# Performance work log

Hardware: AMD Instinct MI355X
Metric: run time of the kernel (lower is better)

The kernel has to match this reference:

```python
import jax, jax.numpy as jnp
import numpy as np
import math

B, S, D_IN, D_ATTN, D_HID = 4, 2048, 1024, 1024, 1024

def gelu_erf(x):
    return 0.5 * x * (1.0 + jax.lax.erf(x / math.sqrt(2.0)))

def setup_inputs() -> dict:
    key = jax.random.key(0)
    k = jax.random.split(key, 8)
    inputs = jax.random.normal(k[0], (B, S, D_IN), dtype=jnp.float32)
    attn_mask = jax.random.randint(k[1], (B, S, S), 0, 2, dtype=jnp.int32)
    sq = 1.0 / math.sqrt(D_IN)
    Wq = jax.random.normal(k[2], (D_IN, D_ATTN), dtype=jnp.float32) * sq
    bq = jnp.zeros((D_ATTN,), dtype=jnp.float32)
    Wk = jax.random.normal(k[3], (D_IN, D_ATTN), dtype=jnp.float32) * sq
    bk = jnp.zeros((D_ATTN,), dtype=jnp.float32)
    Wv = jax.random.normal(k[4], (D_IN, D_HID), dtype=jnp.float32) * sq
    bv = jnp.zeros((D_HID,), dtype=jnp.float32)
    return {"inputs": inputs, "attn_mask": attn_mask,
            "Wq": Wq, "bq": bq, "Wk": Wk, "bk": bk, "Wv": Wv, "bv": bv}

def reference(inputs, attn_mask, Wq, bq, Wk, bk, Wv, bv):
    # Q, K: [B, S, d_k]
    Q = inputs @ Wq + bq
    K = inputs @ Wk + bk
    scores = jnp.einsum('bqd,bkd->bqk', Q, K) / math.sqrt(D_ATTN)
    scores = scores + attn_mask.astype(scores.dtype) * (-1e9)
    attn = jax.nn.softmax(scores, axis=-1)
    WV = gelu_erf(inputs @ Wv + bv)           # [B, S, hidden]
    context = jnp.einsum('bqk,bkh->bqh', attn, WV)
    return (context, attn)
```

## Files before the change

### kernel.cpp

```cpp
#include <hip/hip_runtime.h>
#include <hip/hip_bf16.h>
#include <math.h>

#define B_   4
#define S_   2048
#define DIN  1024
#define DATT 1024
#define DHID 1024

typedef short bf16x8 __attribute__((ext_vector_type(8)));
typedef float f32x4  __attribute__((ext_vector_type(4)));

__device__ inline unsigned short f2bf(float f) {
    unsigned u = __float_as_uint(f);
    u += 0x7fffu + ((u >> 16) & 1u);
    return (unsigned short)(u >> 16);
}
__device__ inline float bf2f(unsigned u16) {
    return __uint_as_float(u16 << 16);
}
__device__ inline void gld16(const void* g, void* l) {
    __builtin_amdgcn_global_load_lds(
        (const __attribute__((address_space(1))) unsigned int*)g,
        (__attribute__((address_space(3))) unsigned int*)l, 16, 0, 0);
}

__global__ __launch_bounds__(256)
void xcvt_k(const float* __restrict__ x, unsigned short* __restrict__ xb)
{
    int i = blockIdx.x * 256 + threadIdx.x;
    const float4* p = (const float4*)x + (size_t)i * 2;
    float4 v0 = p[0], v1 = p[1];
    uint4 o;
    o.x = (unsigned)f2bf(v0.x) | ((unsigned)f2bf(v0.y) << 16);
    o.y = (unsigned)f2bf(v0.z) | ((unsigned)f2bf(v0.w) << 16);
    o.z = (unsigned)f2bf(v1.x) | ((unsigned)f2bf(v1.y) << 16);
    o.w = (unsigned)f2bf(v1.z) | ((unsigned)f2bf(v1.w) << 16);
    ((uint4*)xb)[i] = o;
}

__global__ __launch_bounds__(256)
void wcvt_k(const float* __restrict__ Wq, const float* __restrict__ Wk,
            const float* __restrict__ Wv, unsigned short* __restrict__ Wt)
{
    int w = blockIdx.y;
    const float* W = (w == 0) ? Wq : ((w == 1) ? Wk : Wv);
    unsigned short* D = Wt + (size_t)w * DIN * DATT;
    int t = blockIdx.x * 256 + threadIdx.x;
    int n  = t >> 6;
    int kc = (t & 63) * 16;
    unsigned short r[16];
#pragma unroll
    for (int i = 0; i < 16; ++i) r[i] = f2bf(W[(size_t)(kc + i) * DATT + n]);
    uint4 o0, o1;
    o0.x = (unsigned)r[0] | ((unsigned)r[1] << 16);  o0.y = (unsigned)r[2] | ((unsigned)r[3] << 16);
    o0.z = (unsigned)r[4] | ((unsigned)r[5] << 16);  o0.w = (unsigned)r[6] | ((unsigned)r[7] << 16);
    o1.x = (unsigned)r[8] | ((unsigned)r[9] << 16);  o1.y = (unsigned)r[10] | ((unsigned)r[11] << 16);
    o1.z = (unsigned)r[12] | ((unsigned)r[13] << 16); o1.w = (unsigned)r[14] | ((unsigned)r[15] << 16);
    *(uint4*)(D + (size_t)n * DIN + kc)     = o0;
    *(uint4*)(D + (size_t)n * DIN + kc + 8) = o1;
}

template<int AMODE, int EPI>
__global__ __launch_bounds__(256)
void gemm_k(const void* __restrict__ Ap, const unsigned short* __restrict__ Bp,
            const float* __restrict__ b0, const float* __restrict__ b1,
            const float* __restrict__ b2, const int* __restrict__ maskp,
            void* __restrict__ Cp, void* __restrict__ Cp2,
            int K, int lda, int ldb, int ldc,
            long aStride, long bStride, long cStride, long mStride, float scale)
{
    __shared__ __align__(16) unsigned short sh[2][2][128][64];

    const int tid  = threadIdx.x;
    const int z    = blockIdx.z;
    const int row0 = blockIdx.y * 128;
    const int col0 = blockIdx.x * 128;
    const int wave = tid >> 6, lane = tid & 63;
    const int lr = lane & 15, lg = lane >> 4;
    const int wm = (wave >> 1) * 64, wn = (wave & 1) * 64;

    const unsigned short* Bb = Bp + (size_t)bStride * z;

    f32x4 acc[4][4] = {};
    const int nt = K >> 6;

    auto stage = [&](int b, int k0) {
        if (AMODE == 0) {
            const unsigned short* A = (const unsigned short*)Ap + (size_t)aStride * z;
#pragma unroll
            for (int q = 0; q < 4; ++q) {
                int c = q * 256 + tid;
                int row = c >> 3, j = c & 7;
                gld16((const char*)(A + (size_t)(row0 + row) * lda + k0) + ((j ^ (row & 7)) << 4),
                      (char*)&sh[b][0][0][0] + ((q * 256 + (tid & 192)) << 4));
            }
        } else {
            const float* A = (const float*)Ap + (size_t)aStride * z;
#pragma unroll
            for (int q = 0; q < 4; ++q) {
                int c = q * 256 + tid;
                int row = c >> 3, j = c & 7;
                const float* src = A + (size_t)(row0 + row) * lda + k0 + ((j ^ (row & 7)) << 3);
                float4 v0 = *(const float4*)src;
                float4 v1 = *(const float4*)(src + 4);
                uint4 p;
                p.x = (unsigned)f2bf(v0.x) | ((unsigned)f2bf(v0.y) << 16);
                p.y = (unsigned)f2bf(v0.z) | ((unsigned)f2bf(v0.w) << 16);
                p.z = (unsigned)f2bf(v1.x) | ((unsigned)f2bf(v1.y) << 16);
                p.w = (unsigned)f2bf(v1.z) | ((unsigned)f2bf(v1.w) << 16);
                *(uint4*)((char*)&sh[b][0][0][0] + ((size_t)c << 4)) = p;
            }
        }
#pragma unroll
        for (int q = 0; q < 4; ++q) {
            int c = q * 256 + tid;
            int row = c >> 3, j = c & 7;
            gld16((const char*)(Bb + (size_t)(col0 + row) * ldb + k0) + ((j ^ (row & 7)) << 4),
                  (char*)&sh[b][1][0][0] + ((q * 256 + (tid & 192)) << 4));
        }
    };

    stage(0, 0);
    __syncthreads();
    int cur = 0;
    for (int t = 0; t < nt; ++t) {
        if (t + 1 < nt) stage(cur ^ 1, (t + 1) << 6);
        const char* baseA = (const char*)&sh[cur][0][0][0];
        const char* baseB = (const char*)&sh[cur][1][0][0];
        bf16x8 af[2][4], bfv[2][4];
#pragma unroll
        for (int s = 0; s < 2; ++s)
#pragma unroll
            for (int i = 0; i < 4; ++i) {
                int ra = wm + i * 16 + lr;
                af[s][i]  = *(const bf16x8*)(baseA + ra * 128 + ((((s << 2) | lg) ^ (ra & 7)) << 4));
                int rb = wn + i * 16 + lr;
                bfv[s][i] = *(const bf16x8*)(baseB + rb * 128 + ((((s << 2) | lg) ^ (rb & 7)) << 4));
            }
#pragma unroll
        for (int s = 0; s < 2; ++s)
#pragma unroll
            for (int mi = 0; mi < 4; ++mi)
#pragma unroll
                for (int ni = 0; ni < 4; ++ni)
                    acc[mi][ni] = __builtin_amdgcn_mfma_f32_16x16x32_bf16(af[s][mi], bfv[s][ni], acc[mi][ni], 0, 0, 0);
        if (t + 1 < nt) __syncthreads();
        cur ^= 1;
    }

    if (EPI == 6) {
        int w = col0 >> 10;
        int cb = (col0 & 1023) + wn;
        if (w < 2) {
            unsigned short* C = (unsigned short*)Cp + (size_t)w * ((size_t)B_ * S_ * DATT);
            const float* bias = w ? b1 : b0;
#pragma unroll
            for (int mi = 0; mi < 4; ++mi)
#pragma unroll
                for (int ni = 0; ni < 4; ++ni) {
                    int col = cb + ni * 16 + lr;
                    float bb = bias[col];
                    int rowb = row0 + wm + mi * 16 + lg * 4;
#pragma unroll
                    for (int v = 0; v < 4; ++v)
                        C[(size_t)(rowb + v) * DATT + col] = f2bf(acc[mi][ni][v] + bb);
                }
        } else {
            unsigned short* C = (unsigned short*)Cp2;
            int zz = row0 >> 11;
            int sb = (row0 & 2047) + wm;
#pragma unroll
            for (int mi = 0; mi < 4; ++mi)
#pragma unroll
                for (int ni = 0; ni < 4; ++ni) {
                    int col = cb + ni * 16 + lr;
                    float bb = b2[col];
                    unsigned short r[4];
#pragma unroll
                    for (int v = 0; v < 4; ++v) {
                        float xv = acc[mi][ni][v] + bb;
                        xv = 0.5f * xv * (1.0f + erff(xv * 0.70710678118654752f));
                        r[v] = f2bf(xv);
                    }
                    uint2 o;
                    o.x = (unsigned)r[0] | ((unsigned)r[1] << 16);
                    o.y = (unsigned)r[2] | ((unsigned)r[3] << 16);
                    *(uint2*)(C + ((size_t)zz * DHID + col) * S_ + sb + mi * 16 + lg * 4) = o;
                }
        }
    } else if (EPI == 4) {
        unsigned short* C = (unsigned short*)Cp + (size_t)cStride * z;
        const int* mp = maskp + (size_t)mStride * z;
#pragma unroll
        for (int mi = 0; mi < 4; ++mi)
#pragma unroll
            for (int ni = 0; ni < 4; ++ni) {
                int col = col0 + wn + ni * 16 + lr;
                int rowb = row0 + wm + mi * 16 + lg * 4;
#pragma unroll
                for (int v = 0; v < 4; ++v) {
                    float sv = acc[mi][ni][v] * scale;
                    int mk = mp[(size_t)(rowb + v) * ldc + col];
                    float ev = mk ? 0.0f : __expf(sv);
                    C[(size_t)(rowb + v) * ldc + col] = f2bf(ev);
                }
            }
    } else if (EPI == 5) {
        float* C = (float*)Cp + (size_t)cStride * z;
        const float* invs = b0 + (size_t)z * S_;
#pragma unroll
        for (int mi = 0; mi < 4; ++mi)
#pragma unroll
            for (int ni = 0; ni < 4; ++ni) {
                int col = col0 + wn + ni * 16 + lr;
                int rowb = row0 + wm + mi * 16 + lg * 4;
#pragma unroll
                for (int v = 0; v < 4; ++v)
                    C[(size_t)(rowb + v) * ldc + col] = acc[mi][ni][v] * invs[rowb + v];
            }
    } else {
        float* C = (float*)Cp + (size_t)cStride * z;
        const int* mp = (EPI == 2) ? (maskp + (size_t)mStride * z) : nullptr;
#pragma unroll
        for (int mi = 0; mi < 4; ++mi)
#pragma unroll
            for (int ni = 0; ni < 4; ++ni) {
                int col = col0 + wn + ni * 16 + lr;
                int rowb = row0 + wm + mi * 16 + lg * 4;
#pragma unroll
                for (int v = 0; v < 4; ++v) {
                    float val = acc[mi][ni][v];
                    if (EPI == 2) val = val * scale + (float)mp[(size_t)(rowb + v) * ldc + col] * (-1e9f);
                    C[(size_t)(rowb + v) * ldc + col] = val;
                }
            }
    }
}

template<bool WRITEATTN>
__global__ __launch_bounds__(256)
void rownorm_k(const unsigned short* __restrict__ e, float* __restrict__ attn,
               float* __restrict__ invs)
{
    const int row = blockIdx.x;
    const int tid = threadIdx.x;
    uint4 u = ((const uint4*)(e + (size_t)row * S_))[tid];
    float f[8];
    f[0] = bf2f(u.x & 0xffffu); f[1] = bf2f(u.x >> 16);
    f[2] = bf2f(u.y & 0xffffu); f[3] = bf2f(u.y >> 16);
    f[4] = bf2f(u.z & 0xffffu); f[5] = bf2f(u.z >> 16);
    f[6] = bf2f(u.w & 0xffffu); f[7] = bf2f(u.w >> 16);
    float s = ((f[0] + f[1]) + (f[2] + f[3])) + ((f[4] + f[5]) + (f[6] + f[7]));
#pragma unroll
    for (int o = 32; o; o >>= 1) s += __shfl_xor(s, o);
    __shared__ float red[4];
    if ((tid & 63) == 0) red[tid >> 6] = s;
    __syncthreads();
    s = (red[0] + red[1]) + (red[2] + red[3]);
    float inv = 1.0f / s;
    if (WRITEATTN) {
        float* p = attn + (size_t)row * S_;
        ((float4*)p)[tid * 2]     = make_float4(f[0] * inv, f[1] * inv, f[2] * inv, f[3] * inv);
        ((float4*)p)[tid * 2 + 1] = make_float4(f[4] * inv, f[5] * inv, f[6] * inv, f[7] * inv);
    } else {
        if (tid == 0) invs[row] = inv;
    }
}

__global__ __launch_bounds__(256)
void softmax_k(float* __restrict__ attn)
{
    const int row = blockIdx.x;
    float* p = attn + (size_t)row * S_;
    const int tid = threadIdx.x;
    float4 a = ((const float4*)p)[tid * 2];
    float4 b = ((const float4*)p)[tid * 2 + 1];
    float m = fmaxf(fmaxf(fmaxf(a.x, a.y), fmaxf(a.z, a.w)),
                    fmaxf(fmaxf(b.x, b.y), fmaxf(b.z, b.w)));
#pragma unroll
    for (int o = 32; o; o >>= 1) m = fmaxf(m, __shfl_xor(m, o));
    __shared__ float redm[4];
    __shared__ float reds[4];
    if ((tid & 63) == 0) redm[tid >> 6] = m;
    __syncthreads();
    m = fmaxf(fmaxf(redm[0], redm[1]), fmaxf(redm[2], redm[3]));
    float e[8];
    e[0] = expf(a.x - m); e[1] = expf(a.y - m); e[2] = expf(a.z - m); e[3] = expf(a.w - m);
    e[4] = expf(b.x - m); e[5] = expf(b.y - m); e[6] = expf(b.z - m); e[7] = expf(b.w - m);
    float s = e[0] + e[1] + e[2] + e[3] + e[4] + e[5] + e[6] + e[7];
#pragma unroll
    for (int o = 32; o; o >>= 1) s += __shfl_xor(s, o);
    if ((tid & 63) == 0) reds[tid >> 6] = s;
    __syncthreads();
    s = reds[0] + reds[1] + reds[2] + reds[3];
    float inv = 1.0f / s;
    ((float4*)p)[tid * 2]     = make_float4(e[0] * inv, e[1] * inv, e[2] * inv, e[3] * inv);
    ((float4*)p)[tid * 2 + 1] = make_float4(e[4] * inv, e[5] * inv, e[6] * inv, e[7] * inv);
}

extern "C" void kernel_launch(void* const* d_in, const int* in_sizes, int n_in,
                              void* d_out, int out_size, void* d_ws, size_t ws_size,
                              hipStream_t stream)
{
    const float* x    = (const float*)d_in[0];
    const int*   mask = (const int*)d_in[1];
    const float* Wq   = (const float*)d_in[2];
    const float* bq   = (const float*)d_in[3];
    const float* Wk   = (const float*)d_in[4];
    const float* bk   = (const float*)d_in[5];
    const float* Wv   = (const float*)d_in[6];
    const float* bv   = (const float*)d_in[7];

    float* ctx  = (float*)d_out;
    float* attn = ctx + (size_t)B_ * S_ * DHID;

    unsigned short* Qb = (unsigned short*)ctx;
    unsigned short* Kb = Qb + (size_t)B_ * S_ * DATT;
    unsigned short* Xb   = (unsigned short*)attn;
    unsigned short* Wb   = Xb + (size_t)B_ * S_ * DIN;
    unsigned short* WVbT = Wb + (size_t)3 * DIN * DATT;

    const size_t eElems = (size_t)B_ * S_ * S_;
    bool fast = ws_size >= eElems * 2 + (size_t)B_ * S_ * 4 + 256;

    dim3 blk(256);

    xcvt_k<<<dim3(4096), blk, 0, stream>>>(x, Xb);
    wcvt_k<<<dim3(256, 3), blk, 0, stream>>>(Wq, Wk, Wv, Wb);

    if (fast) {
        unsigned short* e    = (unsigned short*)d_ws;
        float*          invs = (float*)(e + eElems);

        gemm_k<0, 6><<<dim3(24, 64, 1), blk, 0, stream>>>(
            Xb, Wb, bq, bk, bv, nullptr, Qb, WVbT,
            DIN, DIN, DIN, 0, 0, 0, 0, 0, 1.0f);
        gemm_k<0, 4><<<dim3(16, 16, 4), blk, 0, stream>>>(
            Qb, Kb, nullptr, nullptr, nullptr, mask, e, nullptr,
            DATT, DATT, DATT, S_,
            (long)S_ * DATT, (long)S_ * DATT, (long)S_ * S_, (long)S_ * S_, 0.03125f);
        rownorm_k<false><<<dim3(B_ * S_), blk, 0, stream>>>(e, nullptr, invs);
        gemm_k<0, 5><<<dim3(8, 16, 4), blk, 0, stream>>>(
            e, WVbT, invs, nullptr, nullptr, nullptr, ctx, nullptr,
            S_, S_, S_, DHID,
            (long)S_ * S_, (long)DHID * S_, (long)S_ * DHID, 0, 1.0f);
        rownorm_k<true><<<dim3(B_ * S_), blk, 0, stream>>>(e, attn, nullptr);
    } else {
        unsigned short* WVw = (unsigned short*)d_ws;
        gemm_k<0, 6><<<dim3(24, 64, 1), blk, 0, stream>>>(
            Xb, Wb, bq, bk, bv, nullptr, Qb, WVw,
            DIN, DIN, DIN, 0, 0, 0, 0, 0, 1.0f);
        gemm_k<0, 2><<<dim3(16, 16, 4), blk, 0, stream>>>(
            Qb, Kb, nullptr, nullptr, nullptr, mask, attn, nullptr,
            DATT, DATT, DATT, S_,
            (long)S_ * DATT, (long)S_ * DATT, (long)S_ * S_, (long)S_ * S_, 0.03125f);
        softmax_k<<<dim3(B_ * S_), blk, 0, stream>>>(attn);
        gemm_k<1, 3><<<dim3(8, 16, 4), blk, 0, stream>>>(
            attn, WVw, nullptr, nullptr, nullptr, nullptr, ctx, nullptr,
            S_, S_, S_, DHID,
            (long)S_ * S_, (long)DHID * S_, (long)S_ * DHID, 0, 1.0f);
    }
}
```

Measured before the change: 228.5 us.

## Add 256x256-tile, 8-wave GEMM kernel with phased LDS pipelining for fast path

Introduces a new GEMM kernel with 256x256 output tiles, 512 threads and 128KB of LDS double buffering. The main loop is split into four phases that interleave global-to-LDS prefetch with MFMA work, using explicit vmcnt waits, barriers and setprio. All three GEMMs on the fast path (QKV projection, masked exp scores, context) now use it, raising data reuse per loaded tile and reducing global traffic. The trade-off is fewer blocks (e.g. 256 for the score GEMM) and heavy register and LDS use, which can cut occupancy and leave CUs underused at wave tails.

```diff
diff --git a/kernel.cpp b/kernel.cpp
--- a/kernel.cpp
+++ b/kernel.cpp
@@ -61,6 +61,205 @@
     *(uint4*)(D + (size_t)n * DIN + kc + 8) = o1;
 }
 
+template<int EPI>
+__global__ __launch_bounds__(512, 2)
+void gemm256_k(const unsigned short* __restrict__ Ap, const unsigned short* __restrict__ Bp,
+               const float* __restrict__ b0, const float* __restrict__ b1,
+               const float* __restrict__ b2, const int* __restrict__ maskp,
+               void* __restrict__ Cp, void* __restrict__ Cp2,
+               int K, int lda, int ldb, int ldc,
+               long aStride, long bStride, long cStride, long mStride, float scale)
+{
+    __shared__ __align__(16) char ldsb[131072];
+
+    const int tid  = threadIdx.x;
+    const int z    = blockIdx.z;
+    const int row0 = blockIdx.y * 256;
+    const int col0 = blockIdx.x * 256;
+    const int wid  = tid >> 6, lane = tid & 63;
+    const int lr = lane & 15, lg = lane >> 4;
+    const int wm = wid >> 2, wn = wid & 3;
+    const int tw = (tid & 448) * 16;
+
+    const unsigned short* Ab = Ap + (size_t)aStride * z;
+    const unsigned short* Bb = Bp + (size_t)bStride * z;
+
+    const int swzA = lr & 7;
+    const int swzB = lg ^ ((lr >> 1) & 3);
+
+    f32x4 acc[8][4] = {};
+    const int nt = K >> 6;
+
+#define STAGE_A(buf, k0n, r) {                                                  \
+    int gr = (((r) & 1) << 7) + (((r) >> 1) << 6) + (tid >> 3);                 \
+    int jj = (tid & 7) ^ (gr & 7);                                              \
+    gld16(Ab + (size_t)(row0 + gr) * lda + (k0n) + jj * 8,                      \
+          ldsb + (size_t)(buf) * 65536 + (r) * 8192 + tw); }
+
+#define STAGE_B(buf, k0n, r) {                                                  \
+    int rw = (((r) & 1) << 7) + (tid >> 2);                                     \
+    int jj = (tid & 3) ^ ((rw >> 1) & 3);                                       \
+    gld16(Bb + (size_t)(col0 + rw) * ldb + (k0n) + ((r) >> 1) * 32 + jj * 8,    \
+          ldsb + (size_t)(buf) * 65536 + 32768 + ((r) >> 1) * 16384             \
+               + (((r) & 1) << 13) + tw); }
+
+#define PHASE(mh, kk, DOSTAGE) {                                                \
+    const char* lb = ldsb + (size_t)cb * 65536;                                 \
+    bf16x8 av[4], bv[4];                                                        \
+    _Pragma("unroll")                                                           \
+    for (int m = 0; m < 4; ++m) {                                               \
+        int Rl = (mh) * 128 + wm * 64 + m * 16 + lr;                            \
+        av[m] = *(const bf16x8*)(lb + Rl * 128 + ((((kk) * 4 + lg) ^ swzA) * 16)); \
+    }                                                                           \
+    _Pragma("unroll")                                                           \
+    for (int n = 0; n < 4; ++n) {                                               \
+        int Rb = wn * 64 + n * 16 + lr;                                         \
+        bv[n] = *(const bf16x8*)(lb + 32768 + (kk) * 16384 + Rb * 64 + swzB * 16); \
+    }                                                                           \
+    DOSTAGE;                                                                    \
+    asm volatile("s_waitcnt lgkmcnt(0)" ::: "memory");                          \
+    __builtin_amdgcn_sched_barrier(0);                                          \
+    __builtin_amdgcn_s_setprio(1);                                              \
+    _Pragma("unroll")                                                           \
+    for (int m = 0; m < 4; ++m)                                                 \
+        _Pragma("unroll")                                                       \
+        for (int n = 0; n < 4; ++n)                                             \
+            acc[(mh) * 4 + m][n] = __builtin_amdgcn_mfma_f32_16x16x32_bf16(     \
+                av[m], bv[n], acc[(mh) * 4 + m][n], 0, 0, 0);                   \
+    __builtin_amdgcn_s_setprio(0); }
+
+    STAGE_A(0, 0, 0); STAGE_B(0, 0, 0);
+    STAGE_A(0, 0, 1); STAGE_B(0, 0, 1);
+    STAGE_A(0, 0, 2); STAGE_A(0, 0, 3);
+    STAGE_B(0, 0, 2); STAGE_B(0, 0, 3);
+
+    int cb = 0;
+    for (int t = 0; t < nt; ++t) {
+        const bool pf = (t + 1) < nt;
+        const int k0n = (t + 1) << 6;
+        const int nb = cb ^ 1;
+        asm volatile("s_waitcnt vmcnt(4)\ns_barrier" ::: "memory");
+        PHASE(0, 0, if (pf) { STAGE_A(nb, k0n, 0); STAGE_B(nb, k0n, 0); })
+        if (pf) asm volatile("s_waitcnt vmcnt(4)\ns_barrier" ::: "memory");
+        else    asm volatile("s_waitcnt vmcnt(2)\ns_barrier" ::: "memory");
+        PHASE(1, 0, if (pf) { STAGE_A(nb, k0n, 1); STAGE_B(nb, k0n, 1); })
+        if (pf) asm volatile("s_waitcnt vmcnt(4)\ns_barrier" ::: "memory");
+        else    asm volatile("s_waitcnt vmcnt(0)\ns_barrier" ::: "memory");
+        PHASE(0, 1, if (pf) { STAGE_A(nb, k0n, 2); STAGE_A(nb, k0n, 3); })
+        PHASE(1, 1, if (pf) { STAGE_B(nb, k0n, 2); STAGE_B(nb, k0n, 3); })
+        cb = nb;
+    }
+#undef PHASE
+#undef STAGE_A
+#undef STAGE_B
+
+    if (EPI == 6) {
+        int w = col0 >> 10;
+        int cb0 = (col0 & 1023) + wn * 64;
+        if (w < 2) {
+            unsigned short* C = (unsigned short*)Cp + (size_t)w * ((size_t)B_ * S_ * DATT);
+            const float* bias = w ? b1 : b0;
+#pragma unroll
+            for (int ni = 0; ni < 4; ++ni) {
+                int col = cb0 + ni * 16 + lr;
+                float bb = bias[col];
+#pragma unroll
+                for (int mi = 0; mi < 8; ++mi) {
+                    int rowb = row0 + wm * 128 + mi * 16 + lg * 4;
+#pragma unroll
+                    for (int v = 0; v < 4; ++v)
+                        C[(size_t)(rowb + v) * DATT + col] = f2bf(acc[mi][ni][v] + bb);
+                }
+            }
+        } else {
+            unsigned short* C = (unsigned short*)Cp2;
+            int zz = row0 >> 11;
+            int sb = (row0 & 2047) + wm * 128;
+#pragma unroll
+            for (int ni = 0; ni < 4; ++ni) {
+                int col = cb0 + ni * 16 + lr;
+                float bb = b2[col];
+#pragma unroll
+                for (int mi = 0; mi < 8; ++mi) {
+                    unsigned short r[4];
+#pragma unroll
+                    for (int v = 0; v < 4; ++v) {
+                        float xv = acc[mi][ni][v] + bb;
+                        xv = 0.5f * xv * (1.0f + erff(xv * 0.70710678118654752f));
+                        r[v] = f2bf(xv);
+                    }
+                    uint2 o;
+                    o.x = (unsigned)r[0] | ((unsigned)r[1] << 16);
+                    o.y = (unsigned)r[2] | ((unsigned)r[3] << 16);
+                    *(uint2*)(C + ((size_t)zz * DHID + col) * S_ + sb + mi * 16 + lg * 4) = o;
+                }
+            }
+        }
+    } else if (EPI == 4) {
+        unsigned short* C = (unsigned short*)Cp + (size_t)cStride * z;
+        const int* mp = maskp + (size_t)mStride * z;
+#pragma unroll
+        for (int mi = 0; mi < 8; ++mi) {
+            int rowb = row0 + wm * 128 + mi * 16 + lg * 4;
+#pragma unroll
+            for (int ni = 0; ni < 4; ++ni) {
+                int col = col0 + wn * 64 + ni * 16 + lr;
+#pragma unroll
+                for (int v = 0; v < 4; ++v) {
+                    float sv = acc[mi][ni][v] * scale;
+                    int mk = mp[(size_t)(rowb + v) * ldc + col];
+                    float ev = mk ? 0.0f : __expf(sv);
+                    C[(size_t)(rowb + v) * ldc + col] = f2bf(ev);
+                }
+            }
+        }
+    } else {
+        float* C = (float*)Cp + (size_t)cStride * z;
+        const float* invs = b0 + (size_t)z * S_;
+#pragma unroll
+        for (int mi = 0; mi < 8; ++mi) {
+            int rowb = row0 + wm * 128 + mi * 16 + lg * 4;
+#pragma unroll
+            for (int ni = 0; ni < 4; ++ni) {
+                int col = col0 + wn * 64 + ni * 16 + lr;
+#pragma unroll
+                for (int v = 0; v < 4; ++v)
+                    C[(size_t)(rowb + v) * ldc + col] = acc[mi][ni][v] * invs[rowb + v];
+            }
+        }
+    }
+}
+
+template<bool WRITEATTN>
+__global__ __launch_bounds__(256)
+void rownorm_k(const unsigned short* __restrict__ e, float* __restrict__ attn,
+               float* __restrict__ invs)
+{
+    const int row = blockIdx.x;
+    const int tid = threadIdx.x;
+    uint4 u = ((const uint4*)(e + (size_t)row * S_))[tid];
+    float f[8];
+    f[0] = bf2f(u.x & 0xffffu); f[1] = bf2f(u.x >> 16);
+    f[2] = bf2f(u.y & 0xffffu); f[3] = bf2f(u.y >> 16);
+    f[4] = bf2f(u.z & 0xffffu); f[5] = bf2f(u.z >> 16);
+    f[6] = bf2f(u.w & 0xffffu); f[7] = bf2f(u.w >> 16);
+    float s = ((f[0] + f[1]) + (f[2] + f[3])) + ((f[4] + f[5]) + (f[6] + f[7]));
+#pragma unroll
+    for (int o = 32; o; o >>= 1) s += __shfl_xor(s, o);
+    __shared__ float red[4];
+    if ((tid & 63) == 0) red[tid >> 6] = s;
+    __syncthreads();
+    s = (red[0] + red[1]) + (red[2] + red[3]);
+    float inv = 1.0f / s;
+    if (WRITEATTN) {
+        float* p = attn + (size_t)row * S_;
+        ((float4*)p)[tid * 2]     = make_float4(f[0] * inv, f[1] * inv, f[2] * inv, f[3] * inv);
+        ((float4*)p)[tid * 2 + 1] = make_float4(f[4] * inv, f[5] * inv, f[6] * inv, f[7] * inv);
+    } else {
+        if (tid == 0) invs[row] = inv;
+    }
+}
+
 template<int AMODE, int EPI>
 __global__ __launch_bounds__(256)
 void gemm_k(const void* __restrict__ Ap, const unsigned short* __restrict__ Bp,
@@ -71,7 +270,6 @@
             long aStride, long bStride, long cStride, long mStride, float scale)
 {
     __shared__ __align__(16) unsigned short sh[2][2][128][64];
-
     const int tid  = threadIdx.x;
     const int z    = blockIdx.z;
     const int row0 = blockIdx.y * 128;
@@ -79,12 +277,9 @@
     const int wave = tid >> 6, lane = tid & 63;
     const int lr = lane & 15, lg = lane >> 4;
     const int wm = (wave >> 1) * 64, wn = (wave & 1) * 64;
-
     const unsigned short* Bb = Bp + (size_t)bStride * z;
-
     f32x4 acc[4][4] = {};
     const int nt = K >> 6;
-
     auto stage = [&](int b, int k0) {
         if (AMODE == 0) {
             const unsigned short* A = (const unsigned short*)Ap + (size_t)aStride * z;
@@ -120,7 +315,6 @@
                   (char*)&sh[b][1][0][0] + ((q * 256 + (tid & 192)) << 4));
         }
     };
-
     stage(0, 0);
     __syncthreads();
     int cur = 0;
@@ -148,7 +342,6 @@
         if (t + 1 < nt) __syncthreads();
         cur ^= 1;
     }
-
     if (EPI == 6) {
         int w = col0 >> 10;
         int cb = (col0 & 1023) + wn;
@@ -189,36 +382,6 @@
                     *(uint2*)(C + ((size_t)zz * DHID + col) * S_ + sb + mi * 16 + lg * 4) = o;
                 }
         }
-    } else if (EPI == 4) {
-        unsigned short* C = (unsigned short*)Cp + (size_t)cStride * z;
-        const int* mp = maskp + (size_t)mStride * z;
-#pragma unroll
-        for (int mi = 0; mi < 4; ++mi)
-#pragma unroll
-            for (int ni = 0; ni < 4; ++ni) {
-                int col = col0 + wn + ni * 16 + lr;
-                int rowb = row0 + wm + mi * 16 + lg * 4;
-#pragma unroll
-                for (int v = 0; v < 4; ++v) {
-                    float sv = acc[mi][ni][v] * scale;
-                    int mk = mp[(size_t)(rowb + v) * ldc + col];
-                    float ev = mk ? 0.0f : __expf(sv);
-                    C[(size_t)(rowb + v) * ldc + col] = f2bf(ev);
-                }
-            }
-    } else if (EPI == 5) {
-        float* C = (float*)Cp + (size_t)cStride * z;
-        const float* invs = b0 + (size_t)z * S_;
-#pragma unroll
-        for (int mi = 0; mi < 4; ++mi)
-#pragma unroll
-            for (int ni = 0; ni < 4; ++ni) {
-                int col = col0 + wn + ni * 16 + lr;
-                int rowb = row0 + wm + mi * 16 + lg * 4;
-#pragma unroll
-                for (int v = 0; v < 4; ++v)
-                    C[(size_t)(rowb + v) * ldc + col] = acc[mi][ni][v] * invs[rowb + v];
-            }
     } else {
         float* C = (float*)Cp + (size_t)cStride * z;
         const int* mp = (EPI == 2) ? (maskp + (size_t)mStride * z) : nullptr;
@@ -235,36 +398,6 @@
                     C[(size_t)(rowb + v) * ldc + col] = val;
                 }
             }
-    }
-}
-
-template<bool WRITEATTN>
-__global__ __launch_bounds__(256)
-void rownorm_k(const unsigned short* __restrict__ e, float* __restrict__ attn,
-               float* __restrict__ invs)
-{
-    const int row = blockIdx.x;
-    const int tid = threadIdx.x;
-    uint4 u = ((const uint4*)(e + (size_t)row * S_))[tid];
-    float f[8];
-    f[0] = bf2f(u.x & 0xffffu); f[1] = bf2f(u.x >> 16);
-    f[2] = bf2f(u.y & 0xffffu); f[3] = bf2f(u.y >> 16);
-    f[4] = bf2f(u.z & 0xffffu); f[5] = bf2f(u.z >> 16);
-    f[6] = bf2f(u.w & 0xffffu); f[7] = bf2f(u.w >> 16);
-    float s = ((f[0] + f[1]) + (f[2] + f[3])) + ((f[4] + f[5]) + (f[6] + f[7]));
-#pragma unroll
-    for (int o = 32; o; o >>= 1) s += __shfl_xor(s, o);
-    __shared__ float red[4];
-    if ((tid & 63) == 0) red[tid >> 6] = s;
-    __syncthreads();
-    s = (red[0] + red[1]) + (red[2] + red[3]);
-    float inv = 1.0f / s;
-    if (WRITEATTN) {
-        float* p = attn + (size_t)row * S_;
-        ((float4*)p)[tid * 2]     = make_float4(f[0] * inv, f[1] * inv, f[2] * inv, f[3] * inv);
-        ((float4*)p)[tid * 2 + 1] = make_float4(f[4] * inv, f[5] * inv, f[6] * inv, f[7] * inv);
-    } else {
-        if (tid == 0) invs[row] = inv;
     }
 }
 
@@ -324,7 +457,7 @@
     const size_t eElems = (size_t)B_ * S_ * S_;
     bool fast = ws_size >= eElems * 2 + (size_t)B_ * S_ * 4 + 256;
 
-    dim3 blk(256);
+    dim3 blk(256), blk5(512);
 
     xcvt_k<<<dim3(4096), blk, 0, stream>>>(x, Xb);
     wcvt_k<<<dim3(256, 3), blk, 0, stream>>>(Wq, Wk, Wv, Wb);
@@ -333,15 +466,15 @@
         unsigned short* e    = (unsigned short*)d_ws;
         float*          invs = (float*)(e + eElems);
 
-        gemm_k<0, 6><<<dim3(24, 64, 1), blk, 0, stream>>>(
+        gemm256_k<6><<<dim3(12, 32, 1), blk5, 0, stream>>>(
             Xb, Wb, bq, bk, bv, nullptr, Qb, WVbT,
             DIN, DIN, DIN, 0, 0, 0, 0, 0, 1.0f);
-        gemm_k<0, 4><<<dim3(16, 16, 4), blk, 0, stream>>>(
+        gemm256_k<4><<<dim3(8, 8, 4), blk5, 0, stream>>>(
             Qb, Kb, nullptr, nullptr, nullptr, mask, e, nullptr,
             DATT, DATT, DATT, S_,
             (long)S_ * DATT, (long)S_ * DATT, (long)S_ * S_, (long)S_ * S_, 0.03125f);
         rownorm_k<false><<<dim3(B_ * S_), blk, 0, stream>>>(e, nullptr, invs);
-        gemm_k<0, 5><<<dim3(8, 16, 4), blk, 0, stream>>>(
+        gemm256_k<5><<<dim3(4, 8, 4), blk5, 0, stream>>>(
             e, WVbT, invs, nullptr, nullptr, nullptr, ctx, nullptr,
             S_, S_, S_, DHID,
             (long)S_ * S_, (long)DHID * S_, (long)S_ * DHID, 0, 1.0f);
```

Result: slower. 243.0 us (+6.4%).
